# Optimization experiments

Measured on AMD Instinct MI355X. Metric: run time of the kernel, lower is better.

Reference implementation:

```python
import jax, jax.numpy as jnp
import numpy as np

N_NODES = 50000
N_EDGES = 400000
N_TRAIN = 50000
IN_DIM = 128
HIDDEN = 512


def gcn_conv(x, W, b, src, dst, num_nodes):
    """PyG-style GCNConv: linear -> add self-loops -> sym-normalized scatter-add -> bias."""
    h = x @ W  # [N, out]
    loop = jnp.arange(num_nodes, dtype=src.dtype)
    src2 = jnp.concatenate([src, loop])  # self-loops appended
    dst2 = jnp.concatenate([dst, loop])
    ones = jnp.ones(src2.shape[0], dtype=h.dtype)
    deg = jax.ops.segment_sum(ones, dst2, num_segments=num_nodes)  # in-degree incl. self-loop
    dis = jnp.where(deg > 0, jax.lax.rsqrt(deg), 0.0)
    norm = dis[src2] * dis[dst2]  # [E+N]
    msgs = h[src2] * norm[:, None]  # [E+N, out] gather
    out = jax.ops.segment_sum(msgs, dst2, num_segments=num_nodes)  # scatter-add
    return out + b


def setup_inputs() -> dict:
    key = jax.random.key(0)
    ks = jax.random.split(key, 12)
    x = jax.random.normal(ks[0], (N_NODES, IN_DIM), dtype=jnp.float32)
    edge_index = jax.random.randint(ks[1], (2, N_EDGES), 0, N_NODES, dtype=jnp.int32)
    train_edge_id = jax.random.randint(ks[2], (N_TRAIN,), 0, N_EDGES, dtype=jnp.int32)
    def glorot(k, fi, fo):
        s = (6.0 / (fi + fo)) ** 0.5
        return jax.random.uniform(k, (fi, fo), jnp.float32, -s, s)
    return {
        "x": x,
        "edge_index": edge_index,
        "train_edge_id": train_edge_id,
        "W1": glorot(ks[3], IN_DIM, HIDDEN), "b1": jnp.zeros((HIDDEN,), jnp.float32),
        "W2": glorot(ks[4], HIDDEN, HIDDEN), "b2": jnp.zeros((HIDDEN,), jnp.float32),
        "W3": glorot(ks[5], HIDDEN, HIDDEN), "b3": jnp.zeros((HIDDEN,), jnp.float32),
        "fc2_W": glorot(ks[6], HIDDEN, 1), "fc2_b": jnp.zeros((1,), jnp.float32),
    }


def reference(x, edge_index, train_edge_id, W1, b1, W2, b2, W3, b3, fc2_W, fc2_b):
    src, dst = edge_index[0], edge_index[1]
    n = x.shape[0]
    h = jnp.tanh(gcn_conv(x, W1, b1, src, dst, n))
    h = jnp.tanh(gcn_conv(h, W2, b2, src, dst, n))
    h = jnp.tanh(gcn_conv(h, W3, b3, src, dst, n))
    # dropout is identity in eval mode
    node_id = edge_index[:, train_edge_id]  # [2, T]
    e = h[node_id[0]] * h[node_id[1]]  # [T, HIDDEN] edge gather + mul
    return e @ fc2_W + fc2_b  # [T, 1]
```

## Files before the change

kernel.cpp:

```cpp
#include <hip/hip_runtime.h>
#include <math.h>

#define N_NODES 50000
#define N_EDGES 400000
#define N_TRAIN 50000
#define IN_DIM  128
#define HIDDEN  512
#define M_PAD   50048
#define SCAN_B  196

typedef _Float16 f16;
typedef __attribute__((ext_vector_type(8))) _Float16 f16x8;
typedef __attribute__((ext_vector_type(4))) _Float16 f16x4;
typedef __attribute__((ext_vector_type(4))) float f32x4;


__global__ void count_dst_kernel(const int* __restrict__ dst, int* __restrict__ cnt) {
    int i = blockIdx.x * blockDim.x + threadIdx.x;
    if (i < N_EDGES) atomicAdd(&cnt[dst[i]], 1);
}

__global__ void dis_kernel(const int* __restrict__ cnt, float* __restrict__ dis) {
    int v = blockIdx.x * blockDim.x + threadIdx.x;
    if (v < N_NODES) dis[v] = rsqrtf(1.0f + (float)cnt[v]);
}

__global__ void scan1_kernel(const int* __restrict__ cnt, int* __restrict__ bsum) {
    __shared__ int red[256];
    int t = threadIdx.x, i = blockIdx.x * 256 + t;
    red[t] = (i < N_NODES) ? cnt[i] : 0;
    __syncthreads();
    for (int o = 128; o > 0; o >>= 1) {
        if (t < o) red[t] += red[t + o];
        __syncthreads();
    }
    if (t == 0) bsum[blockIdx.x] = red[0];
}

__global__ void scan2_kernel(const int* __restrict__ bsum, int* __restrict__ boff) {
    __shared__ int part[256];
    int t = threadIdx.x;
    int v = (t < SCAN_B) ? bsum[t] : 0;
    part[t] = v;
    __syncthreads();
    for (int o = 1; o < 256; o <<= 1) {
        int u = (t >= o) ? part[t - o] : 0;
        __syncthreads();
        part[t] += u;
        __syncthreads();
    }
    if (t < SCAN_B) boff[t] = part[t] - v;
}

__global__ void scan3_kernel(const int* __restrict__ cnt, const int* __restrict__ boff,
                             int* __restrict__ off) {
    __shared__ int part[256];
    int t = threadIdx.x, i = blockIdx.x * 256 + t;
    int v = (i < N_NODES) ? cnt[i] : 0;
    part[t] = v;
    __syncthreads();
    for (int o = 1; o < 256; o <<= 1) {
        int u = (t >= o) ? part[t - o] : 0;
        __syncthreads();
        part[t] += u;
        __syncthreads();
    }
    int excl = part[t] - v;
    int base = boff[blockIdx.x];
    if (i < N_NODES) off[i] = base + excl;
    if (i == N_NODES - 1) off[N_NODES] = base + excl + v;
}

__global__ void fill_csr_kernel(const int* __restrict__ src, const int* __restrict__ dst,
                                const int* __restrict__ off, int* __restrict__ cursor,
                                const float* __restrict__ dis,
                                int* __restrict__ csr_src, float* __restrict__ csr_w) {
    int i = blockIdx.x * blockDim.x + threadIdx.x;
    if (i < N_EDGES) {
        int d = dst[i], s = src[i];
        int p = atomicAdd(&cursor[d], 1);
        int idx = off[d] + p;
        csr_src[idx] = s;
        csr_w[idx] = dis[s];
    }
}

__global__ void convw_kernel(const float* __restrict__ W, f16* __restrict__ Bt, int K) {
    int idx = blockIdx.x * blockDim.x + threadIdx.x;
    if (idx >= K * HIDDEN) return;
    int k = idx / HIDDEN, n = idx % HIDDEN;
    float w = W[(size_t)k * HIDDEN + n];
    f16 hi = (f16)w;
    f16 lo = (f16)(w - (float)hi);
    size_t base = (size_t)n * 2 * K;
    Bt[base + k]     = hi;
    Bt[base + K + k] = lo;
}

__global__ void agg1_kernel(const float* __restrict__ x, const float* __restrict__ dis,
                            const int* __restrict__ off, const int* __restrict__ csr_src,
                            const float* __restrict__ csr_w, f16* __restrict__ A) {
    const int TPN = 32;
    int node = blockIdx.x * 8 + threadIdx.x / TPN;
    if (node >= N_NODES) return;
    int t = threadIdx.x % TPN;
    float dv = dis[node];
    float w0 = dv * dv;
    float4 a = ((const float4*)(x + (size_t)node * IN_DIM))[t];
    float4 acc = make_float4(a.x * w0, a.y * w0, a.z * w0, a.w * w0);
    float4 acc1 = make_float4(0.f, 0.f, 0.f, 0.f);
    int s0 = off[node], s1 = off[node + 1];
    int k = s0;
    for (; k + 2 <= s1; k += 2) {
        int sa = csr_src[k], sb = csr_src[k + 1];
        float wa = csr_w[k] * dv, wb = csr_w[k + 1] * dv;
        float4 ba = ((const float4*)(x + (size_t)sa * IN_DIM))[t];
        float4 bb = ((const float4*)(x + (size_t)sb * IN_DIM))[t];
        acc.x = fmaf(wa, ba.x, acc.x);   acc.y = fmaf(wa, ba.y, acc.y);
        acc.z = fmaf(wa, ba.z, acc.z);   acc.w = fmaf(wa, ba.w, acc.w);
        acc1.x = fmaf(wb, bb.x, acc1.x); acc1.y = fmaf(wb, bb.y, acc1.y);
        acc1.z = fmaf(wb, bb.z, acc1.z); acc1.w = fmaf(wb, bb.w, acc1.w);
    }
    if (k < s1) {
        int sa = csr_src[k];
        float wa = csr_w[k] * dv;
        float4 ba = ((const float4*)(x + (size_t)sa * IN_DIM))[t];
        acc.x = fmaf(wa, ba.x, acc.x); acc.y = fmaf(wa, ba.y, acc.y);
        acc.z = fmaf(wa, ba.z, acc.z); acc.w = fmaf(wa, ba.w, acc.w);
    }
    f16x4 o;
    o.x = (f16)(acc.x + acc1.x); o.y = (f16)(acc.y + acc1.y);
    o.z = (f16)(acc.z + acc1.z); o.w = (f16)(acc.w + acc1.w);
    *(f16x4*)&A[(size_t)node * IN_DIM + t * 4] = o;
}

__global__ void agg_f16_kernel(const f16* __restrict__ h, const float* __restrict__ dis,
                               const int* __restrict__ off, const int* __restrict__ csr_src,
                               const float* __restrict__ csr_w, f16* __restrict__ A) {
    const int TPN = 64;
    int node = blockIdx.x * 4 + threadIdx.x / TPN;
    if (node >= N_NODES) return;
    int t = threadIdx.x % TPN;
    float dv = dis[node];
    float w0 = dv * dv;
    f16x8 a = *(const f16x8*)&h[(size_t)node * HIDDEN + t * 8];
    float acc0[8], acc1[8];
    #pragma unroll
    for (int j = 0; j < 8; j++) { acc0[j] = w0 * (float)a[j]; acc1[j] = 0.f; }
    int s0 = off[node], s1 = off[node + 1];
    int k = s0;
    for (; k + 4 <= s1; k += 4) {
        int sa = csr_src[k],     sb = csr_src[k + 1];
        int sc = csr_src[k + 2], sd = csr_src[k + 3];
        float wa = csr_w[k] * dv,     wb = csr_w[k + 1] * dv;
        float wc = csr_w[k + 2] * dv, wd = csr_w[k + 3] * dv;
        f16x8 ba = *(const f16x8*)&h[(size_t)sa * HIDDEN + t * 8];
        f16x8 bb = *(const f16x8*)&h[(size_t)sb * HIDDEN + t * 8];
        f16x8 bc = *(const f16x8*)&h[(size_t)sc * HIDDEN + t * 8];
        f16x8 bd = *(const f16x8*)&h[(size_t)sd * HIDDEN + t * 8];
        #pragma unroll
        for (int j = 0; j < 8; j++) {
            acc0[j] = fmaf(wa, (float)ba[j], acc0[j]);
            acc1[j] = fmaf(wb, (float)bb[j], acc1[j]);
            acc0[j] = fmaf(wc, (float)bc[j], acc0[j]);
            acc1[j] = fmaf(wd, (float)bd[j], acc1[j]);
        }
    }
    for (; k < s1; k++) {
        int sa = csr_src[k];
        float wa = csr_w[k] * dv;
        f16x8 ba = *(const f16x8*)&h[(size_t)sa * HIDDEN + t * 8];
        #pragma unroll
        for (int j = 0; j < 8; j++) acc0[j] = fmaf(wa, (float)ba[j], acc0[j]);
    }
    f16x8 o;
    #pragma unroll
    for (int j = 0; j < 8; j++) o[j] = (f16)(acc0[j] + acc1[j]);
    *(f16x8*)&A[(size_t)node * HIDDEN + t * 8] = o;
}

__global__ __launch_bounds__(256, 3) void gemm_mfma_kernel(
    const f16* __restrict__ A, const f16* __restrict__ Bt, const float* __restrict__ bias,
    f16* __restrict__ C, int M, int Kb) {
    __shared__ f16 smem[24576];
    f16* As  = smem;
    f16* Bs0 = smem + 8192;
    const int Kp = 2 * Kb;
    int tid = threadIdx.x;
    int lane = tid & 63, wv = tid >> 6;
    int wr = wv >> 1, wc = wv & 1;

    int nwg = gridDim.x;
    int q = nwg >> 3, r = nwg & 7;
    int xcd = blockIdx.x & 7, pos = blockIdx.x >> 3;
    int wgid = (xcd < r ? xcd * (q + 1) : r * (q + 1) + (xcd - r) * q) + pos;
    int j0 = (wgid & 3) * 128;
    int i0 = (wgid >> 2) * 128;

    int l15 = lane & 15, l4 = lane >> 4;

    f32x4 acc[4][4];
    #pragma unroll
    for (int m = 0; m < 4; m++)
        #pragma unroll
        for (int n = 0; n < 4; n++)
            acc[m][n] = (f32x4){0.f, 0.f, 0.f, 0.f};

    const int nt = Kb / 64;
    for (int t = 0; t < nt; t++) {
        int k0 = t * 64;
        if (t) __syncthreads();
        #pragma unroll
        for (int i = 0; i < 4; i++) {
            int s = i * 256 + tid;
            int row = s >> 3, c8 = s & 7;
            int c8s = c8 ^ (row & 7);
            const f16* gp = A + (size_t)(i0 + row) * Kb + k0 + c8s * 8;
            f16* lp = &As[(i * 256 + wv * 64) * 8];
            __builtin_amdgcn_global_load_lds(
                (const __attribute__((address_space(1))) void*)gp,
                (__attribute__((address_space(3))) void*)lp, 16, 0, 0);
        }
        #pragma unroll
        for (int v = 0; v < 2; v++)
            #pragma unroll
            for (int i = 0; i < 4; i++) {
                int s = i * 256 + tid;
                int row = s >> 3, c8 = s & 7;
                int c8s = c8 ^ (row & 7);
                const f16* gp = Bt + (size_t)(j0 + row) * Kp + v * Kb + k0 + c8s * 8;
                f16* lp = &Bs0[(v * 1024 + i * 256 + wv * 64) * 8];
                __builtin_amdgcn_global_load_lds(
                    (const __attribute__((address_space(1))) void*)gp,
                    (__attribute__((address_space(3))) void*)lp, 16, 0, 0);
            }
        __syncthreads();

        f16x8 af[4][2], bfr[4][2][2];
        #pragma unroll
        for (int m = 0; m < 4; m++) {
            int row = wr * 64 + m * 16 + l15;
            #pragma unroll
            for (int kk = 0; kk < 2; kk++) {
                int slot = (kk * 4 + l4) ^ (row & 7);
                af[m][kk] = *(const f16x8*)&As[row * 64 + slot * 8];
            }
        }
        #pragma unroll
        for (int n = 0; n < 4; n++) {
            int brow = wc * 64 + n * 16 + l15;
            #pragma unroll
            for (int v = 0; v < 2; v++)
                #pragma unroll
                for (int kk = 0; kk < 2; kk++) {
                    int slot = (kk * 4 + l4) ^ (brow & 7);
                    bfr[n][v][kk] = *(const f16x8*)&Bs0[v * 8192 + brow * 64 + slot * 8];
                }
        }
        #pragma unroll
        for (int m = 0; m < 4; m++)
            #pragma unroll
            for (int n = 0; n < 4; n++)
                #pragma unroll
                for (int v = 0; v < 2; v++)
                    #pragma unroll
                    for (int kk = 0; kk < 2; kk++)
                        acc[m][n] = __builtin_amdgcn_mfma_f32_16x16x32_f16(
                            af[m][kk], bfr[n][v][kk], acc[m][n], 0, 0, 0);
    }

    __syncthreads();
    #pragma unroll
    for (int m = 0; m < 4; m++) {
        #pragma unroll
        for (int n = 0; n < 4; n++) {
            int lcol = wc * 64 + n * 16 + l15;
            float bc = bias[j0 + lcol];
            #pragma unroll
            for (int rr = 0; rr < 4; rr++) {
                int lrow = wr * 64 + m * 16 + l4 * 4 + rr;
                smem[lrow * 136 + lcol] = (f16)tanhf(acc[m][n][rr] + bc);
            }
        }
    }
    __syncthreads();
    #pragma unroll
    for (int j = 0; j < 8; j++) {
        int qq = j * 256 + tid;
        int row = qq >> 4, c8 = qq & 15;
        int grow = i0 + row;
        if (grow < M)
            *(f16x8*)&C[(size_t)grow * HIDDEN + j0 + c8 * 8] =
                *(const f16x8*)&smem[row * 136 + c8 * 8];
    }
}

__global__ void edge_score_kernel(const f16* __restrict__ h,
                                  const int* __restrict__ src, const int* __restrict__ dst,
                                  const int* __restrict__ te, const float* __restrict__ wgt,
                                  const float* __restrict__ fc2b, float* __restrict__ out) {
    int wid = threadIdx.x / 64;
    int lane = threadIdx.x % 64;
    int e = blockIdx.x * 4 + wid;
    if (e >= N_TRAIN) return;
    int id = te[e];
    int a = src[id], b = dst[id];
    f16x8 ha = *(const f16x8*)&h[(size_t)a * HIDDEN + lane * 8];
    f16x8 hb = *(const f16x8*)&h[(size_t)b * HIDDEN + lane * 8];
    float4 w0 = *(const float4*)&wgt[lane * 8];
    float4 w1 = *(const float4*)&wgt[lane * 8 + 4];
    float acc = 0.f;
    acc += (float)ha[0] * (float)hb[0] * w0.x;
    acc += (float)ha[1] * (float)hb[1] * w0.y;
    acc += (float)ha[2] * (float)hb[2] * w0.z;
    acc += (float)ha[3] * (float)hb[3] * w0.w;
    acc += (float)ha[4] * (float)hb[4] * w1.x;
    acc += (float)ha[5] * (float)hb[5] * w1.y;
    acc += (float)ha[6] * (float)hb[6] * w1.z;
    acc += (float)ha[7] * (float)hb[7] * w1.w;
    #pragma unroll
    for (int o = 32; o > 0; o >>= 1) acc += __shfl_down(acc, o);
    if (lane == 0) out[e] = acc + fc2b[0];
}


extern "C" void kernel_launch(void* const* d_in, const int* in_sizes, int n_in,
                              void* d_out, int out_size, void* d_ws, size_t ws_size,
                              hipStream_t stream) {
    const float* x    = (const float*)d_in[0];
    const int*   eidx = (const int*)d_in[1];
    const int*   te   = (const int*)d_in[2];
    const float* W1   = (const float*)d_in[3];
    const float* b1   = (const float*)d_in[4];
    const float* W2   = (const float*)d_in[5];
    const float* b2   = (const float*)d_in[6];
    const float* W3   = (const float*)d_in[7];
    const float* b3   = (const float*)d_in[8];
    const float* fc2W = (const float*)d_in[9];
    const float* fc2b = (const float*)d_in[10];
    const int* srcp = eidx;
    const int* dstp = eidx + N_EDGES;

    char* ws = (char*)d_ws;
    size_t used = 0;
    auto alloc = [&](size_t bytes) {
        void* p = ws + used;
        used += (bytes + 255) / 256 * 256;
        return p;
    };
    int*   cnt     = (int*)alloc((size_t)N_NODES * 4);
    int*   off     = (int*)alloc((size_t)(N_NODES + 1) * 4);
    int*   cursor  = (int*)alloc((size_t)N_NODES * 4);
    int*   bsum    = (int*)alloc((size_t)SCAN_B * 4);
    int*   boff    = (int*)alloc((size_t)SCAN_B * 4);
    int*   csr_src = (int*)alloc((size_t)N_EDGES * 4);
    float* csr_w   = (float*)alloc((size_t)N_EDGES * 4);
    float* dis     = (float*)alloc((size_t)N_NODES * 4);
    f16* Bt1 = (f16*)alloc((size_t)HIDDEN * 2 * IN_DIM * 2);
    f16* Bt2 = (f16*)alloc((size_t)HIDDEN * 2 * HIDDEN * 2);
    f16* Bt3 = (f16*)alloc((size_t)HIDDEN * 2 * HIDDEN * 2);
    f16* GA  = (f16*)alloc((size_t)M_PAD * HIDDEN * 2);
    f16* F   = (f16*)alloc((size_t)M_PAD * HIDDEN * 2);

    if (used > ws_size) return;

    hipMemsetAsync(cnt, 0, (size_t)N_NODES * 4, stream);
    hipMemsetAsync(cursor, 0, (size_t)N_NODES * 4, stream);

    count_dst_kernel<<<(N_EDGES + 255) / 256, 256, 0, stream>>>(dstp, cnt);
    dis_kernel<<<(N_NODES + 255) / 256, 256, 0, stream>>>(cnt, dis);
    scan1_kernel<<<SCAN_B, 256, 0, stream>>>(cnt, bsum);
    scan2_kernel<<<1, 256, 0, stream>>>(bsum, boff);
    scan3_kernel<<<SCAN_B, 256, 0, stream>>>(cnt, boff, off);
    fill_csr_kernel<<<(N_EDGES + 255) / 256, 256, 0, stream>>>(srcp, dstp, off, cursor, dis,
                                                               csr_src, csr_w);

    convw_kernel<<<(IN_DIM * HIDDEN + 255) / 256, 256, 0, stream>>>(W1, Bt1, IN_DIM);
    convw_kernel<<<(HIDDEN * HIDDEN + 255) / 256, 256, 0, stream>>>(W2, Bt2, HIDDEN);
    convw_kernel<<<(HIDDEN * HIDDEN + 255) / 256, 256, 0, stream>>>(W3, Bt3, HIDDEN);

    int gemm_blocks = (HIDDEN / 128) * (M_PAD / 128);

    agg1_kernel<<<(N_NODES + 7) / 8, 256, 0, stream>>>(x, dis, off, csr_src, csr_w, GA);
    gemm_mfma_kernel<<<gemm_blocks, 256, 0, stream>>>(GA, Bt1, b1, F, N_NODES, IN_DIM);
    agg_f16_kernel<<<(N_NODES + 3) / 4, 256, 0, stream>>>(F, dis, off, csr_src, csr_w, GA);
    gemm_mfma_kernel<<<gemm_blocks, 256, 0, stream>>>(GA, Bt2, b2, F, N_NODES, HIDDEN);
    agg_f16_kernel<<<(N_NODES + 3) / 4, 256, 0, stream>>>(F, dis, off, csr_src, csr_w, GA);
    gemm_mfma_kernel<<<gemm_blocks, 256, 0, stream>>>(GA, Bt3, b3, F, N_NODES, HIDDEN);
    edge_score_kernel<<<(N_TRAIN + 3) / 4, 256, 0, stream>>>(F, srcp, dstp, te, fc2W, fc2b,
                                                             (float*)d_out);
}
```

Before: 417.7 us.

## Drop split-f16 weight residual in GEMM and deepen aggregation gather unroll

Weights were stored as an f16 hi and lo pair, which doubled the MFMA work and the B-tile loads. They are now a single f16 value, halving the GEMM compute and B traffic and shrinking shared memory so occupancy can rise to 4 blocks per SM. The f16 aggregation loop now issues 8 neighbor gathers per iteration instead of 4, to keep more memory loads in flight. The cost is lower weight precision in the GEMM, plus more registers used in the aggregation kernel.

```diff
diff --git a/kernel.cpp b/kernel.cpp
--- a/kernel.cpp
+++ b/kernel.cpp
@@ -89,12 +89,7 @@
     int idx = blockIdx.x * blockDim.x + threadIdx.x;
     if (idx >= K * HIDDEN) return;
     int k = idx / HIDDEN, n = idx % HIDDEN;
-    float w = W[(size_t)k * HIDDEN + n];
-    f16 hi = (f16)w;
-    f16 lo = (f16)(w - (float)hi);
-    size_t base = (size_t)n * 2 * K;
-    Bt[base + k]     = hi;
-    Bt[base + K + k] = lo;
+    Bt[(size_t)n * K + k] = (f16)W[(size_t)k * HIDDEN + n];
 }
 
 __global__ void agg1_kernel(const float* __restrict__ x, const float* __restrict__ dis,
@@ -149,24 +144,58 @@
     for (int j = 0; j < 8; j++) { acc0[j] = w0 * (float)a[j]; acc1[j] = 0.f; }
     int s0 = off[node], s1 = off[node + 1];
     int k = s0;
-    for (; k + 4 <= s1; k += 4) {
-        int sa = csr_src[k],     sb = csr_src[k + 1];
-        int sc = csr_src[k + 2], sd = csr_src[k + 3];
-        float wa = csr_w[k] * dv,     wb = csr_w[k + 1] * dv;
-        float wc = csr_w[k + 2] * dv, wd = csr_w[k + 3] * dv;
+    for (; k + 8 <= s1; k += 8) {
+        f16x8 b[8];
+        float w[8];
+        #pragma unroll
+        for (int u = 0; u < 8; u++) {
+            int su = csr_src[k + u];
+            w[u] = csr_w[k + u] * dv;
+            b[u] = *(const f16x8*)&h[(size_t)su * HIDDEN + t * 8];
+        }
+        #pragma unroll
+        for (int j = 0; j < 8; j++) {
+            acc0[j] = fmaf(w[0], (float)b[0][j], acc0[j]);
+            acc1[j] = fmaf(w[1], (float)b[1][j], acc1[j]);
+            acc0[j] = fmaf(w[2], (float)b[2][j], acc0[j]);
+            acc1[j] = fmaf(w[3], (float)b[3][j], acc1[j]);
+            acc0[j] = fmaf(w[4], (float)b[4][j], acc0[j]);
+            acc1[j] = fmaf(w[5], (float)b[5][j], acc1[j]);
+            acc0[j] = fmaf(w[6], (float)b[6][j], acc0[j]);
+            acc1[j] = fmaf(w[7], (float)b[7][j], acc1[j]);
+        }
+    }
+    if (k + 4 <= s1) {
+        f16x8 b[4];
+        float w[4];
+        #pragma unroll
+        for (int u = 0; u < 4; u++) {
+            int su = csr_src[k + u];
+            w[u] = csr_w[k + u] * dv;
+            b[u] = *(const f16x8*)&h[(size_t)su * HIDDEN + t * 8];
+        }
+        #pragma unroll
+        for (int j = 0; j < 8; j++) {
+            acc0[j] = fmaf(w[0], (float)b[0][j], acc0[j]);
+            acc1[j] = fmaf(w[1], (float)b[1][j], acc1[j]);
+            acc0[j] = fmaf(w[2], (float)b[2][j], acc0[j]);
+            acc1[j] = fmaf(w[3], (float)b[3][j], acc1[j]);
+        }
+        k += 4;
+    }
+    if (k + 2 <= s1) {
+        int sa = csr_src[k], sb = csr_src[k + 1];
+        float wa = csr_w[k] * dv, wb = csr_w[k + 1] * dv;
         f16x8 ba = *(const f16x8*)&h[(size_t)sa * HIDDEN + t * 8];
         f16x8 bb = *(const f16x8*)&h[(size_t)sb * HIDDEN + t * 8];
-        f16x8 bc = *(const f16x8*)&h[(size_t)sc * HIDDEN + t * 8];
-        f16x8 bd = *(const f16x8*)&h[(size_t)sd * HIDDEN + t * 8];
         #pragma unroll
         for (int j = 0; j < 8; j++) {
             acc0[j] = fmaf(wa, (float)ba[j], acc0[j]);
             acc1[j] = fmaf(wb, (float)bb[j], acc1[j]);
-            acc0[j] = fmaf(wc, (float)bc[j], acc0[j]);
-            acc1[j] = fmaf(wd, (float)bd[j], acc1[j]);
-        }
-    }
-    for (; k < s1; k++) {
+        }
+        k += 2;
+    }
+    if (k < s1) {
         int sa = csr_src[k];
         float wa = csr_w[k] * dv;
         f16x8 ba = *(const f16x8*)&h[(size_t)sa * HIDDEN + t * 8];
@@ -179,13 +208,12 @@
     *(f16x8*)&A[(size_t)node * HIDDEN + t * 8] = o;
 }
 
-__global__ __launch_bounds__(256, 3) void gemm_mfma_kernel(
+__global__ __launch_bounds__(256, 4) void gemm_mfma_kernel(
     const f16* __restrict__ A, const f16* __restrict__ Bt, const float* __restrict__ bias,
     f16* __restrict__ C, int M, int Kb) {
-    __shared__ f16 smem[24576];
-    f16* As  = smem;
-    f16* Bs0 = smem + 8192;
-    const int Kp = 2 * Kb;
+    __shared__ f16 smem[17408];
+    f16* As = smem;
+    f16* Bs = smem + 8192;
     int tid = threadIdx.x;
     int lane = tid & 63, wv = tid >> 6;
     int wr = wv >> 1, wc = wv & 1;
@@ -222,21 +250,19 @@
                 (__attribute__((address_space(3))) void*)lp, 16, 0, 0);
         }
         #pragma unroll
-        for (int v = 0; v < 2; v++)
-            #pragma unroll
-            for (int i = 0; i < 4; i++) {
-                int s = i * 256 + tid;
-                int row = s >> 3, c8 = s & 7;
-                int c8s = c8 ^ (row & 7);
-                const f16* gp = Bt + (size_t)(j0 + row) * Kp + v * Kb + k0 + c8s * 8;
-                f16* lp = &Bs0[(v * 1024 + i * 256 + wv * 64) * 8];
-                __builtin_amdgcn_global_load_lds(
-                    (const __attribute__((address_space(1))) void*)gp,
-                    (__attribute__((address_space(3))) void*)lp, 16, 0, 0);
-            }
-        __syncthreads();
-
-        f16x8 af[4][2], bfr[4][2][2];
+        for (int i = 0; i < 4; i++) {
+            int s = i * 256 + tid;
+            int row = s >> 3, c8 = s & 7;
+            int c8s = c8 ^ (row & 7);
+            const f16* gp = Bt + (size_t)(j0 + row) * Kb + k0 + c8s * 8;
+            f16* lp = &Bs[(i * 256 + wv * 64) * 8];
+            __builtin_amdgcn_global_load_lds(
+                (const __attribute__((address_space(1))) void*)gp,
+                (__attribute__((address_space(3))) void*)lp, 16, 0, 0);
+        }
+        __syncthreads();
+
+        f16x8 af[4][2], bfr[4][2];
         #pragma unroll
         for (int m = 0; m < 4; m++) {
             int row = wr * 64 + m * 16 + l15;
@@ -250,23 +276,19 @@
         for (int n = 0; n < 4; n++) {
             int brow = wc * 64 + n * 16 + l15;
             #pragma unroll
-            for (int v = 0; v < 2; v++)
-                #pragma unroll
-                for (int kk = 0; kk < 2; kk++) {
-                    int slot = (kk * 4 + l4) ^ (brow & 7);
-                    bfr[n][v][kk] = *(const f16x8*)&Bs0[v * 8192 + brow * 64 + slot * 8];
-                }
+            for (int kk = 0; kk < 2; kk++) {
+                int slot = (kk * 4 + l4) ^ (brow & 7);
+                bfr[n][kk] = *(const f16x8*)&Bs[brow * 64 + slot * 8];
+            }
         }
         #pragma unroll
         for (int m = 0; m < 4; m++)
             #pragma unroll
             for (int n = 0; n < 4; n++)
                 #pragma unroll
-                for (int v = 0; v < 2; v++)
-                    #pragma unroll
-                    for (int kk = 0; kk < 2; kk++)
-                        acc[m][n] = __builtin_amdgcn_mfma_f32_16x16x32_f16(
-                            af[m][kk], bfr[n][v][kk], acc[m][n], 0, 0, 0);
+                for (int kk = 0; kk < 2; kk++)
+                    acc[m][n] = __builtin_amdgcn_mfma_f32_16x16x32_f16(
+                        af[m][kk], bfr[n][kk], acc[m][n], 0, 0, 0);
     }
 
     __syncthreads();
@@ -356,9 +378,9 @@
     int*   csr_src = (int*)alloc((size_t)N_EDGES * 4);
     float* csr_w   = (float*)alloc((size_t)N_EDGES * 4);
     float* dis     = (float*)alloc((size_t)N_NODES * 4);
-    f16* Bt1 = (f16*)alloc((size_t)HIDDEN * 2 * IN_DIM * 2);
-    f16* Bt2 = (f16*)alloc((size_t)HIDDEN * 2 * HIDDEN * 2);
-    f16* Bt3 = (f16*)alloc((size_t)HIDDEN * 2 * HIDDEN * 2);
+    f16* Bt1 = (f16*)alloc((size_t)HIDDEN * IN_DIM * 2);
+    f16* Bt2 = (f16*)alloc((size_t)HIDDEN * HIDDEN * 2);
+    f16* Bt3 = (f16*)alloc((size_t)HIDDEN * HIDDEN * 2);
     f16* GA  = (f16*)alloc((size_t)M_PAD * HIDDEN * 2);
     f16* F   = (f16*)alloc((size_t)M_PAD * HIDDEN * 2);
 
```

Measured after the change: 357.8 us. 14.3% less time.
